# Kernel optimization log

Hardware: AMD Instinct MI355X
Metric: run time of the kernel (lower is better)

Reference implementation:

```python
import jax, jax.numpy as jnp
import numpy as np


def setup_inputs() -> dict:
    key = jax.random.key(0)
    k1, k2, k3 = jax.random.split(key, 3)
    B, N, F, U = 8, 2048, 128, 128
    A = jax.random.uniform(k1, (B, N, N), dtype=jnp.float32)   # dense nonneg adjacency
    X = jax.random.normal(k2, (B, N, F), dtype=jnp.float32)
    W = jax.random.normal(k3, (F, U), dtype=jnp.float32)
    bias = jnp.zeros((U,), dtype=jnp.float32)
    p = jnp.zeros((1,), dtype=jnp.float32)
    q = jnp.zeros((1,), dtype=jnp.float32)
    return {"A": A, "X": X, "W": W, "bias": bias, "p": p, "q": q}


def reference(A, X, W, bias, p, q):
    # learn_pqr path of MyGCN: A_ = D @ (A + q*I) @ D with D = diag(k^-0.25),
    # k = p + (1-p)*colsum(A). Diag matmuls expressed as broadcasted scaling (same math).
    B, N, _ = A.shape
    ps = jax.nn.sigmoid(p)          # shape (1,)
    qs = jax.nn.sigmoid(q)
    Dr = jnp.sum(A, axis=1)          # [B, N]  (K.sum axis=1)
    k_vec = ps + (1.0 - ps) * Dr     # [B, N]
    k_inv_root = jnp.sqrt(k_vec) ** -0.5   # k^{-0.25}
    k_clean = jnp.where(jnp.isinf(k_inv_root), 0.0, k_inv_root)  # [B, N]
    I = jnp.eye(N, dtype=A.dtype)
    AqI = A + qs[0] * I              # [B, N, N]
    A_ = k_clean[:, :, None] * AqI * k_clean[:, None, :]
    XW = jnp.einsum('bnf,fu->bnu', X, W)        # [B, N, U]
    A_XW = jnp.einsum('bnm,bmu->bnu', A_, XW)   # [B, N, U]
    out = A_XW + bias
    return jax.nn.relu(out)
```

## Files before the change

kernel.cpp:

```cpp
#include <hip/hip_runtime.h>
#include <stdint.h>

#define N 2048
#define F 128
#define UDIM 128

typedef __attribute__((ext_vector_type(8))) __bf16 bf16x8;
typedef __attribute__((ext_vector_type(8))) unsigned short us8;
typedef __attribute__((ext_vector_type(4))) float f32x4;

__device__ __forceinline__ unsigned short f2bf(float f) {
  union { float f; uint32_t u; } v; v.f = f;
  uint32_t u = v.u;
  return (unsigned short)((u + 0x7FFFu + ((u >> 16) & 1u)) >> 16);
}

__device__ __forceinline__ void async_load16(const void* g, void* l) {
  typedef const __attribute__((address_space(1))) uint32_t* gp_t;
  typedef __attribute__((address_space(3))) uint32_t* lp_t;
  __builtin_amdgcn_global_load_lds((gp_t)(uintptr_t)g, (lp_t)(uint32_t)(uintptr_t)l, 16, 0, 0);
}

__global__ __launch_bounds__(256)
void gcn_colsum_conv(const float* __restrict__ A, const float* __restrict__ qptr,
                     const float* __restrict__ W,
                     float* __restrict__ partial, unsigned short* __restrict__ Abf,
                     unsigned short* __restrict__ WTb) {
  const int b = blockIdx.z;
  const int rc = blockIdx.y;
  const int j = blockIdx.x * 1024 + threadIdx.x * 4;
  const float qs = 1.0f / (1.0f + __expf(-qptr[0]));
  const size_t base = (size_t)b * N * N + (size_t)rc * 32 * N + j;
  const float* ap = A + base;
  unsigned short* op = Abf + base;
  const int grow0 = rc * 32;
  float s0 = 0.f, s1 = 0.f, s2 = 0.f, s3 = 0.f;
  #pragma unroll 4
  for (int rr = 0; rr < 32; ++rr) {
    float4 v = *(const float4*)(ap + (size_t)rr * N);
    s0 += v.x; s1 += v.y; s2 += v.z; s3 += v.w;
    const int dj = grow0 + rr - j;
    if (dj == 0) v.x += qs;
    else if (dj == 1) v.y += qs;
    else if (dj == 2) v.z += qs;
    else if (dj == 3) v.w += qs;
    ushort4 o;
    o.x = f2bf(v.x); o.y = f2bf(v.y); o.z = f2bf(v.z); o.w = f2bf(v.w);
    *(ushort4*)(op + (size_t)rr * N) = o;
  }
  float4 s; s.x = s0; s.y = s1; s.z = s2; s.w = s3;
  *(float4*)&partial[((size_t)b * 64 + rc) * N + j] = s;

  if (blockIdx.y == 0 && blockIdx.z == 0) {
    #pragma unroll 4
    for (int it = 0; it < 32; ++it) {
      const int flat = it * 512 + blockIdx.x * 256 + threadIdx.x;
      const int k_ = flat >> 7;
      const int u = flat & 127;
      WTb[u * 128 + k_] = f2bf(W[flat]);
    }
  }
}

__global__ __launch_bounds__(256, 2)
void gcn_xwT(const float* __restrict__ X, const unsigned short* __restrict__ WTb,
             const float* __restrict__ partial, const float* __restrict__ pptr,
             float* __restrict__ kcl, unsigned short* __restrict__ YT) {
  __shared__ __align__(16) unsigned short Wl[128 * 128];
  __shared__ __align__(16) unsigned short Xl[32 * 128];
  __shared__ float red[8][33];
  __shared__ float kct[32];

  const int t = threadIdx.x;
  const int lane = t & 63;
  const int wid = t >> 6;
  const int b = blockIdx.x >> 6;
  const int i0 = (blockIdx.x & 63) << 5;

  #pragma unroll
  for (int rnd = 0; rnd < 8; ++rnd) {
    const int u = rnd * 16 + (t >> 4);
    const int c16 = (t & 15) ^ (u & 7);
    async_load16(WTb + u * 128 + c16 * 8, &Wl[rnd * 2048 + (t & ~63) * 8]);
  }
  {
    const int r = t >> 3;
    const float* xp = X + ((size_t)b * N + i0 + r) * F + (t & 7) * 8;
    #pragma unroll
    for (int h = 0; h < 2; ++h) {
      float4 v0 = *(const float4*)(xp + h * 64);
      float4 v1 = *(const float4*)(xp + h * 64 + 4);
      us8 w;
      w[0] = f2bf(v0.x); w[1] = f2bf(v0.y); w[2] = f2bf(v0.z); w[3] = f2bf(v0.w);
      w[4] = f2bf(v1.x); w[5] = f2bf(v1.y); w[6] = f2bf(v1.z); w[7] = f2bf(v1.w);
      const int slot = (t & 7) + h * 8;
      *(us8*)&Xl[r * 128 + ((slot ^ (r & 7)) * 8)] = w;
    }
  }
  {
    const int col = t & 31;
    const int grp = t >> 5;
    float s = 0.f;
    #pragma unroll
    for (int rr = 0; rr < 8; ++rr)
      s += partial[((size_t)b * 64 + grp * 8 + rr) * N + i0 + col];
    red[grp][col] = s;
  }
  __syncthreads();
  if (t < 32) {
    float s = 0.f;
    #pragma unroll
    for (int g = 0; g < 8; ++g) s += red[g][t];
    const float sp = 1.0f / (1.0f + __expf(-pptr[0]));
    const float k = sp + (1.0f - sp) * s;
    float rv = rsqrtf(sqrtf(k));
    if (isinf(rv)) rv = 0.f;
    kct[t] = rv;
    kcl[b * N + i0 + t] = rv;
  }
  __syncthreads();

  f32x4 acc[2][2];
  #pragma unroll
  for (int a = 0; a < 2; ++a)
    #pragma unroll
    for (int c = 0; c < 2; ++c) { f32x4 z = {0.f, 0.f, 0.f, 0.f}; acc[a][c] = z; }

  const int u0 = wid * 32;
  #pragma unroll
  for (int kc = 0; kc < 4; ++kc) {
    bf16x8 af[2], bfv[2];
    #pragma unroll
    for (int ut = 0; ut < 2; ++ut) {
      const int u = u0 + ut * 16 + (lane & 15);
      const int sl = ((kc * 4 + (lane >> 4)) ^ (u & 7)) * 8;
      af[ut] = *(const bf16x8*)&Wl[u * 128 + sl];
    }
    #pragma unroll
    for (int it = 0; it < 2; ++it) {
      const int rr = it * 16 + (lane & 15);
      const int sl = ((kc * 4 + (lane >> 4)) ^ (rr & 7)) * 8;
      bfv[it] = *(const bf16x8*)&Xl[rr * 128 + sl];
    }
    #pragma unroll
    for (int ut = 0; ut < 2; ++ut)
      #pragma unroll
      for (int it = 0; it < 2; ++it)
        acc[ut][it] = __builtin_amdgcn_mfma_f32_16x16x32_bf16(af[ut], bfv[it], acc[ut][it], 0, 0, 0);
  }

  #pragma unroll
  for (int ut = 0; ut < 2; ++ut) {
    #pragma unroll
    for (int it = 0; it < 2; ++it) {
      const int ic = it * 16 + (lane & 15);
      const float kv = kct[ic];
      #pragma unroll
      for (int rg = 0; rg < 4; ++rg) {
        const int u = u0 + ut * 16 + (lane >> 4) * 4 + rg;
        YT[(size_t)b * UDIM * N + (size_t)u * N + i0 + ic] = f2bf(acc[ut][it][rg] * kv);
      }
    }
  }
}

__global__ __launch_bounds__(256, 2)
void gcn_gemm(const unsigned short* __restrict__ Abf, const unsigned short* __restrict__ YT,
              const float* __restrict__ kcl, const float* __restrict__ bias,
              float* __restrict__ out) {
  __shared__ __align__(16) unsigned short Abuf[3][32 * 64];
  __shared__ __align__(16) unsigned short Ybuf[3][128 * 64];

  const int t = threadIdx.x;
  const int lane = t & 63;
  const int wid = t >> 6;
  const int wr = wid >> 1;
  const int wc = wid & 1;

  const int bid = blockIdx.x;
  const int b = bid & 7;
  const int i0 = (bid >> 3) << 5;

  const int r = t >> 3;
  const int c8 = t & 7;
  const unsigned short* Ab = Abf + (size_t)b * N * N + (size_t)(i0 + r) * N + ((c8 ^ (r & 7)) * 8);
  const unsigned short* YTb = YT + (size_t)b * UDIM * N;

  const int a_wavebase = (t & ~63) * 8;
  const int y_u = t >> 3;
  const int y_wavebase = (t & ~63) * 8;

  f32x4 acc[4];
  #pragma unroll
  for (int i = 0; i < 4; ++i) { f32x4 z = {0.f, 0.f, 0.f, 0.f}; acc[i] = z; }

  auto issue = [&](int kt, int buf) {
    const int k0 = kt * 64;
    #pragma unroll
    for (int rnd = 0; rnd < 4; ++rnd) {
      const int u = rnd * 32 + y_u;
      const int c16 = (t & 7) ^ (u & 7);
      async_load16(YTb + (size_t)u * N + k0 + c16 * 8, &Ybuf[buf][rnd * 2048 + y_wavebase]);
    }
    async_load16(Ab + k0, &Abuf[buf][a_wavebase]);
  };

  auto compute = [&](int cur) {
    #pragma unroll
    for (int kk = 0; kk < 2; ++kk) {
      const int ar = 16 * wr + (lane & 15);
      const int as = ((kk * 4 + (lane >> 4)) ^ (ar & 7)) * 8;
      bf16x8 af = *(const bf16x8*)&Abuf[cur][ar * 64 + as];
      #pragma unroll
      for (int ut = 0; ut < 4; ++ut) {
        const int u = 64 * wc + ut * 16 + (lane & 15);
        const int bs = ((kk * 4 + (lane >> 4)) ^ (u & 7)) * 8;
        bf16x8 bfv = *(const bf16x8*)&Ybuf[cur][u * 64 + bs];
        acc[ut] = __builtin_amdgcn_mfma_f32_16x16x32_bf16(af, bfv, acc[ut], 0, 0, 0);
      }
    }
  };

  issue(0, 0);
  issue(1, 1);

  #pragma unroll 1
  for (int kt0 = 0; kt0 < 30; kt0 += 3) {
    asm volatile("s_waitcnt vmcnt(5)" ::: "memory");
    __builtin_amdgcn_s_barrier();
    __builtin_amdgcn_sched_barrier(0);
    issue(kt0 + 2, 2);
    compute(0);

    asm volatile("s_waitcnt vmcnt(5)" ::: "memory");
    __builtin_amdgcn_s_barrier();
    __builtin_amdgcn_sched_barrier(0);
    issue(kt0 + 3, 0);
    compute(1);

    asm volatile("s_waitcnt vmcnt(5)" ::: "memory");
    __builtin_amdgcn_s_barrier();
    __builtin_amdgcn_sched_barrier(0);
    issue(kt0 + 4, 1);
    compute(2);
  }
  asm volatile("s_waitcnt vmcnt(5)" ::: "memory");
  __builtin_amdgcn_s_barrier();
  __builtin_amdgcn_sched_barrier(0);
  compute(0);
  asm volatile("s_waitcnt vmcnt(0)" ::: "memory");
  __builtin_amdgcn_s_barrier();
  __builtin_amdgcn_sched_barrier(0);
  compute(1);

  const int irow = i0 + 16 * wr + (lane >> 4) * 4;
  #pragma unroll
  for (int ut = 0; ut < 4; ++ut) {
    const int u = 64 * wc + ut * 16 + (lane & 15);
    const float bv = bias[u];
    #pragma unroll
    for (int rg = 0; rg < 4; ++rg) {
      const int i = irow + rg;
      const float kv = kcl[b * N + i];
      float vv = kv * acc[ut][rg] + bv;
      out[((size_t)b * N + i) * UDIM + u] = vv > 0.f ? vv : 0.f;
    }
  }
}

extern "C" void kernel_launch(void* const* d_in, const int* in_sizes, int n_in,
                              void* d_out, int out_size, void* d_ws, size_t ws_size,
                              hipStream_t stream) {
  (void)in_sizes; (void)n_in; (void)out_size; (void)ws_size;
  const float* A    = (const float*)d_in[0];
  const float* X    = (const float*)d_in[1];
  const float* W    = (const float*)d_in[2];
  const float* bias = (const float*)d_in[3];
  const float* p    = (const float*)d_in[4];
  const float* q    = (const float*)d_in[5];
  float* out = (float*)d_out;

  char* ws = (char*)d_ws;
  float* partial      = (float*)ws;
  float* kcl          = (float*)(ws + 4194304);
  unsigned short* WTb = (unsigned short*)(ws + 4194304 + 65536);
  unsigned short* YT  = (unsigned short*)(ws + 4292608);
  unsigned short* Abf = (unsigned short*)(ws + 4292608 + 4194304);

  gcn_colsum_conv<<<dim3(2, 64, 8), dim3(256), 0, stream>>>(A, q, W, partial, Abf, WTb);
  gcn_xwT<<<dim3(512), dim3(256), 0, stream>>>(X, WTb, partial, p, kcl, YT);
  gcn_gemm<<<dim3(512), dim3(256), 0, stream>>>(Abf, YT, kcl, bias, out);
}
```

Measured before the change: 63.11 us.

## Fuse A fp32-to-bf16 conversion into GEMM and fold identity term into epilogue

Removes the intermediate bf16 copy of A: the column-sum kernel now only reads A, and the GEMM loads fp32 A into registers, converts it, and stores it to LDS within its pipeline. The q·I term is applied algebraically in the epilogue by adding qs times the scaled Y row instead of modifying the diagonal of A. This removes a large global write and read, but the GEMM now reads twice as many bytes for A and uses more registers. Its pipeline also shifts from async LDS loads to register staging.

```diff
diff --git a/kernel.cpp b/kernel.cpp
--- a/kernel.cpp
+++ b/kernel.cpp
@@ -14,6 +14,9 @@
   uint32_t u = v.u;
   return (unsigned short)((u + 0x7FFFu + ((u >> 16) & 1u)) >> 16);
 }
+__device__ __forceinline__ float bf2f(unsigned short u) {
+  union { uint32_t u; float f; } v; v.u = ((uint32_t)u) << 16; return v.f;
+}
 
 __device__ __forceinline__ void async_load16(const void* g, void* l) {
   typedef const __attribute__((address_space(1))) uint32_t* gp_t;
@@ -22,31 +25,17 @@
 }
 
 __global__ __launch_bounds__(256)
-void gcn_colsum_conv(const float* __restrict__ A, const float* __restrict__ qptr,
-                     const float* __restrict__ W,
-                     float* __restrict__ partial, unsigned short* __restrict__ Abf,
-                     unsigned short* __restrict__ WTb) {
+void gcn_colsum(const float* __restrict__ A, const float* __restrict__ W,
+                float* __restrict__ partial, unsigned short* __restrict__ WTb) {
   const int b = blockIdx.z;
   const int rc = blockIdx.y;
   const int j = blockIdx.x * 1024 + threadIdx.x * 4;
-  const float qs = 1.0f / (1.0f + __expf(-qptr[0]));
-  const size_t base = (size_t)b * N * N + (size_t)rc * 32 * N + j;
-  const float* ap = A + base;
-  unsigned short* op = Abf + base;
-  const int grow0 = rc * 32;
+  const float* ap = A + (size_t)b * N * N + (size_t)rc * 32 * N + j;
   float s0 = 0.f, s1 = 0.f, s2 = 0.f, s3 = 0.f;
   #pragma unroll 4
   for (int rr = 0; rr < 32; ++rr) {
     float4 v = *(const float4*)(ap + (size_t)rr * N);
     s0 += v.x; s1 += v.y; s2 += v.z; s3 += v.w;
-    const int dj = grow0 + rr - j;
-    if (dj == 0) v.x += qs;
-    else if (dj == 1) v.y += qs;
-    else if (dj == 2) v.z += qs;
-    else if (dj == 3) v.w += qs;
-    ushort4 o;
-    o.x = f2bf(v.x); o.y = f2bf(v.y); o.z = f2bf(v.z); o.w = f2bf(v.w);
-    *(ushort4*)(op + (size_t)rr * N) = o;
   }
   float4 s; s.x = s0; s.y = s1; s.z = s2; s.w = s3;
   *(float4*)&partial[((size_t)b * 64 + rc) * N + j] = s;
@@ -165,9 +154,9 @@
 }
 
 __global__ __launch_bounds__(256, 2)
-void gcn_gemm(const unsigned short* __restrict__ Abf, const unsigned short* __restrict__ YT,
+void gcn_gemm(const float* __restrict__ A, const unsigned short* __restrict__ YT,
               const float* __restrict__ kcl, const float* __restrict__ bias,
-              float* __restrict__ out) {
+              const float* __restrict__ qptr, float* __restrict__ out) {
   __shared__ __align__(16) unsigned short Abuf[3][32 * 64];
   __shared__ __align__(16) unsigned short Ybuf[3][128 * 64];
 
@@ -181,12 +170,14 @@
   const int b = bid & 7;
   const int i0 = (bid >> 3) << 5;
 
+  const float qs = 1.0f / (1.0f + __expf(-qptr[0]));
+
   const int r = t >> 3;
   const int c8 = t & 7;
-  const unsigned short* Ab = Abf + (size_t)b * N * N + (size_t)(i0 + r) * N + ((c8 ^ (r & 7)) * 8);
+  const float* Ap = A + (size_t)b * N * N + (size_t)(i0 + r) * N + c8 * 8;
   const unsigned short* YTb = YT + (size_t)b * UDIM * N;
 
-  const int a_wavebase = (t & ~63) * 8;
+  const int a_woff = r * 64 + ((c8 ^ (r & 7)) * 8);
   const int y_u = t >> 3;
   const int y_wavebase = (t & ~63) * 8;
 
@@ -194,7 +185,13 @@
   #pragma unroll
   for (int i = 0; i < 4; ++i) { f32x4 z = {0.f, 0.f, 0.f, 0.f}; acc[i] = z; }
 
-  auto issue = [&](int kt, int buf) {
+  float4 ar0, ar1;
+
+  auto issueA = [&](int kt) {
+    ar0 = *(const float4*)(Ap + kt * 64);
+    ar1 = *(const float4*)(Ap + kt * 64 + 4);
+  };
+  auto issueY = [&](int kt, int buf) {
     const int k0 = kt * 64;
     #pragma unroll
     for (int rnd = 0; rnd < 4; ++rnd) {
@@ -202,9 +199,13 @@
       const int c16 = (t & 7) ^ (u & 7);
       async_load16(YTb + (size_t)u * N + k0 + c16 * 8, &Ybuf[buf][rnd * 2048 + y_wavebase]);
     }
-    async_load16(Ab + k0, &Abuf[buf][a_wavebase]);
   };
-
+  auto convertA = [&](int buf) {
+    us8 w;
+    w[0] = f2bf(ar0.x); w[1] = f2bf(ar0.y); w[2] = f2bf(ar0.z); w[3] = f2bf(ar0.w);
+    w[4] = f2bf(ar1.x); w[5] = f2bf(ar1.y); w[6] = f2bf(ar1.z); w[7] = f2bf(ar1.w);
+    *(us8*)&Abuf[buf][a_woff] = w;
+  };
   auto compute = [&](int cur) {
     #pragma unroll
     for (int kk = 0; kk < 2; ++kk) {
@@ -221,30 +222,43 @@
     }
   };
 
-  issue(0, 0);
-  issue(1, 1);
+#define STEP(KT, CUR, NXT, ISS)                                  \
+  {                                                              \
+    asm volatile("s_waitcnt vmcnt(4)" ::: "memory");             \
+    convertA(NXT);                                               \
+    asm volatile("s_waitcnt lgkmcnt(0)" ::: "memory");           \
+    __builtin_amdgcn_s_barrier();                                \
+    __builtin_amdgcn_sched_barrier(0);                           \
+    issueA((KT) + 2);                                            \
+    __builtin_amdgcn_sched_barrier(0);                           \
+    issueY((KT) + 2, (ISS));                                     \
+    __builtin_amdgcn_sched_barrier(0);                           \
+    compute(CUR);                                                \
+  }
+
+  issueA(0);
+  __builtin_amdgcn_sched_barrier(0);
+  issueY(0, 0);
+  __builtin_amdgcn_sched_barrier(0);
+  asm volatile("s_waitcnt vmcnt(4)" ::: "memory");
+  convertA(0);
+  __builtin_amdgcn_sched_barrier(0);
+  issueA(1);
+  __builtin_amdgcn_sched_barrier(0);
+  issueY(1, 1);
+  __builtin_amdgcn_sched_barrier(0);
 
   #pragma unroll 1
   for (int kt0 = 0; kt0 < 30; kt0 += 3) {
-    asm volatile("s_waitcnt vmcnt(5)" ::: "memory");
-    __builtin_amdgcn_s_barrier();
-    __builtin_amdgcn_sched_barrier(0);
-    issue(kt0 + 2, 2);
-    compute(0);
-
-    asm volatile("s_waitcnt vmcnt(5)" ::: "memory");
-    __builtin_amdgcn_s_barrier();
-    __builtin_amdgcn_sched_barrier(0);
-    issue(kt0 + 3, 0);
-    compute(1);
-
-    asm volatile("s_waitcnt vmcnt(5)" ::: "memory");
-    __builtin_amdgcn_s_barrier();
-    __builtin_amdgcn_sched_barrier(0);
-    issue(kt0 + 4, 1);
-    compute(2);
-  }
-  asm volatile("s_waitcnt vmcnt(5)" ::: "memory");
+    STEP(kt0,     0, 1, 2);
+    STEP(kt0 + 1, 1, 2, 0);
+    STEP(kt0 + 2, 2, 0, 1);
+  }
+#undef STEP
+
+  asm volatile("s_waitcnt vmcnt(4)" ::: "memory");
+  convertA(1);
+  asm volatile("s_waitcnt lgkmcnt(0)" ::: "memory");
   __builtin_amdgcn_s_barrier();
   __builtin_amdgcn_sched_barrier(0);
   compute(0);
@@ -261,8 +275,9 @@
     #pragma unroll
     for (int rg = 0; rg < 4; ++rg) {
       const int i = irow + rg;
+      const float yv = bf2f(YTb[(size_t)u * N + i]);
       const float kv = kcl[b * N + i];
-      float vv = kv * acc[ut][rg] + bv;
+      float vv = kv * (acc[ut][rg] + qs * yv) + bv;
       out[((size_t)b * N + i) * UDIM + u] = vv > 0.f ? vv : 0.f;
     }
   }
@@ -285,9 +300,8 @@
   float* kcl          = (float*)(ws + 4194304);
   unsigned short* WTb = (unsigned short*)(ws + 4194304 + 65536);
   unsigned short* YT  = (unsigned short*)(ws + 4292608);
-  unsigned short* Abf = (unsigned short*)(ws + 4292608 + 4194304);
-
-  gcn_colsum_conv<<<dim3(2, 64, 8), dim3(256), 0, stream>>>(A, q, W, partial, Abf, WTb);
+
+  gcn_colsum<<<dim3(2, 64, 8), dim3(256), 0, stream>>>(A, W, partial, WTb);
   gcn_xwT<<<dim3(512), dim3(256), 0, stream>>>(X, WTb, partial, p, kcl, YT);
-  gcn_gemm<<<dim3(512), dim3(256), 0, stream>>>(Abf, YT, kcl, bias, out);
-}
+  gcn_gemm<<<dim3(512), dim3(256), 0, stream>>>(A, YT, kcl, bias, q, out);
+}
```

Measured after the change: 62.15 us. About the same (-1.5%).
